# Kernel tuning notes

Hardware: AMD Instinct MI355X
Metric: run time of the kernel (lower is better)

The kernel has to match this reference:

```python
import jax, jax.numpy as jnp
import numpy as np

N = 20000   # nodes
E = 640000  # edges (avg degree 32)
D = 128     # input_nf == output_nf
H = 128     # hidden_size


def silu(x):
    return x * jax.nn.sigmoid(x)


def setup_inputs() -> dict:
    key = jax.random.key(0)
    ks = jax.random.split(key, 16)
    def lin(k, out_d, in_d, scale=None):
        s = scale if scale is not None else (1.0 / np.sqrt(in_d))
        return jax.random.uniform(k, (out_d, in_d), jnp.float32, -s, s)
    return {
        "h": jax.random.normal(ks[0], (N, D), jnp.float32),
        "coord": jax.random.normal(ks[1], (N, 3), jnp.float32),
        "edge_index": jax.random.randint(ks[2], (2, E), 0, N, jnp.int32),
        # edge_mlp: Linear(2D+1 -> H), Linear(H -> H)
        "We1": lin(ks[3], H, 2 * D + 1), "be1": jnp.zeros((H,), jnp.float32),
        "We2": lin(ks[4], H, H),          "be2": jnp.zeros((H,), jnp.float32),
        # node_mlp: Linear(H+D -> H), Linear(H -> D)
        "Wn1": lin(ks[5], H, H + D),      "bn1": jnp.zeros((H,), jnp.float32),
        "Wn2": lin(ks[6], D, H),          "bn2": jnp.zeros((D,), jnp.float32),
        # coord_mlp: Linear(H -> H), Linear(H -> 1, no bias, xavier gain=0.001)
        "Wc1": lin(ks[7], H, H),          "bc1": jnp.zeros((H,), jnp.float32),
        "Wc2": lin(ks[8], 1, H, scale=0.001 * np.sqrt(6.0 / (H + 1))),
    }


def reference(h, coord, edge_index, We1, be1, We2, be2, Wn1, bn1, Wn2, bn2, Wc1, bc1, Wc2):
    src, dst = edge_index[0], edge_index[1]

    # coord2radial (normalize=False)
    coord_diff = coord[src] - coord[dst]                 # [E, 3]
    radial = jnp.sum(coord_diff * coord_diff, axis=1, keepdims=True)  # [E, 1]

    # edge model: cat(h[src], h[dst], radial) -> Lin -> SiLU -> Lin -> SiLU
    e_in = jnp.concatenate([h[src], h[dst], radial], axis=1)  # [E, 2D+1]
    edge_feat = silu(silu(e_in @ We1.T + be1) @ We2.T + be2)  # [E, H]

    # coord model: coord_diff * coord_mlp(edge_feat), scatter-add over src
    w = silu(edge_feat @ Wc1.T + bc1) @ Wc2.T                 # [E, 1]
    trans = coord_diff * w                                    # [E, 3]
    coord_out = coord + jax.ops.segment_sum(trans, src, num_segments=N)

    # node model: agg edge_feat over src, cat(h, agg) -> Lin -> SiLU -> Lin, residual
    agg = jax.ops.segment_sum(edge_feat, src, num_segments=N)  # [N, H]
    n_in = jnp.concatenate([h, agg], axis=1)                   # [N, H+D]
    h_out = h + (silu(n_in @ Wn1.T + bn1) @ Wn2.T + bn2)       # [N, D]

    return (h_out, coord_out)
```

## Files before the change

### kernel.cpp

```cpp
#include <hip/hip_runtime.h>

#define N_NODES 20000
#define N_EDGES 640000
#define D 128
#define H 128

#define EB   128
#define TPB  512
#define NBLK 256
#define NTILE (N_EDGES / EB)
#define NNT  ((N_NODES + EB - 1) / EB)
#define ST   136

#define WS_W1   0
#define WS_W2   65536
#define WS_WC1  98304
#define WS_WN1  131072
#define WS_WN2  196608
#define WS_CNT  229376
#define WS_CUR  309376
#define WS_PERM 389376
#define WS_U    2949376
#define WS_V    8069376
#define WS_P    13189376

typedef short bf16x8 __attribute__((ext_vector_type(8)));
typedef float f32x4  __attribute__((ext_vector_type(4)));

__device__ __forceinline__ float silu_f(float x) {
    return x * __builtin_amdgcn_rcpf(1.0f + __expf(-x));
}
__device__ __forceinline__ ushort f2b(float f) {
    union { float f; unsigned int u; } v; v.f = f;
    return (ushort)((v.u + 0x7FFF + ((v.u >> 16) & 1)) >> 16);
}
__device__ __forceinline__ float b2f(ushort s) {
    union { unsigned int u; float f; } v; v.u = ((unsigned int)s) << 16; return v.f;
}

__device__ __forceinline__ void gemm_chunk_rw(const ushort* Ab, int kc0,
                                              const bf16x8 b[2], f32x4 acc[4][2],
                                              int eg, int lane)
{
    const int r = lane & 15, g = lane >> 4;
    bf16x8 a[4];
    #pragma unroll
    for (int mt = 0; mt < 4; ++mt)
        a[mt] = *(const bf16x8*)&Ab[(eg * 64 + mt * 16 + r) * ST + kc0 + g * 8];
    #pragma unroll
    for (int mt = 0; mt < 4; ++mt)
        #pragma unroll
        for (int nt = 0; nt < 2; ++nt)
            acc[mt][nt] = __builtin_amdgcn_mfma_f32_16x16x32_bf16(a[mt], b[nt], acc[mt][nt], 0, 0, 0);
}

__device__ __forceinline__ void zero_acc8(f32x4 acc[4][2]) {
    #pragma unroll
    for (int mt = 0; mt < 4; ++mt)
        #pragma unroll
        for (int nt = 0; nt < 2; ++nt)
            acc[mt][nt] = (f32x4){0.f, 0.f, 0.f, 0.f};
}

__device__ __forceinline__ void epi_silu8(f32x4 acc[4][2], const float* bias,
                                          ushort* out, int eg, int cg, int lane) {
    const int r = lane & 15, g = lane >> 4;
    #pragma unroll
    for (int nt = 0; nt < 2; ++nt) {
        int o = cg * 32 + nt * 16 + r;
        float bo = bias[o];
        #pragma unroll
        for (int mt = 0; mt < 4; ++mt)
            #pragma unroll
            for (int j = 0; j < 4; ++j) {
                int e = eg * 64 + mt * 16 + g * 4 + j;
                out[e * ST + o] = f2b(silu_f(acc[mt][nt][j] + bo));
            }
    }
}

__global__ void prep(const float* __restrict__ We1, const float* __restrict__ We2,
                     const float* __restrict__ Wc1, const float* __restrict__ Wn1,
                     const float* __restrict__ Wn2, const float* __restrict__ coord,
                     ushort* w1, ushort* w2, ushort* wc1, ushort* wn1, ushort* wn2,
                     int* cnt, float* hout, float* cout)
{
    int idx = blockIdx.x * 256 + threadIdx.x;
    if (idx < 32768) { w1[idx] = f2b(We1[(idx >> 8) * 257 + (idx & 255)]); return; }
    idx -= 32768;
    if (idx < 16384) { w2[idx] = f2b(We2[idx]); return; }
    idx -= 16384;
    if (idx < 16384) { wc1[idx] = f2b(Wc1[idx]); return; }
    idx -= 16384;
    if (idx < 32768) { wn1[idx] = f2b(Wn1[idx]); return; }
    idx -= 32768;
    if (idx < 16384) { wn2[idx] = f2b(Wn2[idx]); return; }
    idx -= 16384;
    if (idx < N_NODES) { cnt[idx] = 0; return; }
    idx -= N_NODES;
    if (idx < N_NODES * D) { hout[idx] = 0.f; return; }
    idx -= N_NODES * D;
    if (idx < N_NODES * 3) cout[idx] = coord[idx];
}

__global__ __launch_bounds__(TPB, 2)
void uvp_k(const float* __restrict__ h,
           const ushort* __restrict__ w1b, const ushort* __restrict__ wn1b,
           const float* __restrict__ be1, const float* __restrict__ bn1,
           ushort* __restrict__ u, ushort* __restrict__ v, ushort* __restrict__ p)
{
    __shared__ __align__(16) ushort hs[EB * ST];
    __shared__ float b1s[H], bn1s[H];

    const int tid = threadIdx.x, lane = tid & 63, wv = tid >> 6;
    const int eg = wv >> 2, cg = wv & 3;
    const int r = lane & 15, g = lane >> 4;
    const int n0 = blockIdx.x * EB;

    if (tid < 128) b1s[tid] = be1[tid];
    else if (tid < 256) bn1s[tid - 128] = bn1[tid - 128];

    bf16x8 wa[4][2], wb[4][2], wn[4][2];
    {
        const int c0 = cg * 32 + r, c1c = c0 + 16;
        #pragma unroll
        for (int kc = 0; kc < 4; ++kc) {
            wa[kc][0] = *(const bf16x8*)&w1b [c0  * 256 +       kc * 32 + g * 8];
            wa[kc][1] = *(const bf16x8*)&w1b [c1c * 256 +       kc * 32 + g * 8];
            wb[kc][0] = *(const bf16x8*)&w1b [c0  * 256 + 128 + kc * 32 + g * 8];
            wb[kc][1] = *(const bf16x8*)&w1b [c1c * 256 + 128 + kc * 32 + g * 8];
            wn[kc][0] = *(const bf16x8*)&wn1b[c0  * 256 +       kc * 32 + g * 8];
            wn[kc][1] = *(const bf16x8*)&wn1b[c1c * 256 +       kc * 32 + g * 8];
        }
    }
    #pragma unroll
    for (int it = 0; it < 8; ++it) {
        int idx = tid + it * TPB;
        int e = idx >> 5, c = idx & 31;
        int n = n0 + e; if (n >= N_NODES) n = 0;
        float4 vv = *(const float4*)&h[(size_t)n * D + c * 4];
        ushort4 pk; pk.x = f2b(vv.x); pk.y = f2b(vv.y); pk.z = f2b(vv.z); pk.w = f2b(vv.w);
        *(ushort4*)&hs[e * ST + c * 4] = pk;
    }
    __syncthreads();

    f32x4 acc[4][2];
    zero_acc8(acc);
    #pragma unroll
    for (int kc = 0; kc < 4; ++kc) gemm_chunk_rw(hs, kc * 32, wa[kc], acc, eg, lane);
    #pragma unroll
    for (int nt = 0; nt < 2; ++nt) {
        int o = cg * 32 + nt * 16 + r;
        float bo = b1s[o];
        #pragma unroll
        for (int mt = 0; mt < 4; ++mt)
            #pragma unroll
            for (int j = 0; j < 4; ++j) {
                int n = n0 + eg * 64 + mt * 16 + g * 4 + j;
                if (n < N_NODES) u[(size_t)n * H + o] = f2b(acc[mt][nt][j] + bo);
            }
    }
    zero_acc8(acc);
    #pragma unroll
    for (int kc = 0; kc < 4; ++kc) gemm_chunk_rw(hs, kc * 32, wb[kc], acc, eg, lane);
    #pragma unroll
    for (int nt = 0; nt < 2; ++nt) {
        int o = cg * 32 + nt * 16 + r;
        #pragma unroll
        for (int mt = 0; mt < 4; ++mt)
            #pragma unroll
            for (int j = 0; j < 4; ++j) {
                int n = n0 + eg * 64 + mt * 16 + g * 4 + j;
                if (n < N_NODES) v[(size_t)n * H + o] = f2b(acc[mt][nt][j]);
            }
    }
    zero_acc8(acc);
    #pragma unroll
    for (int kc = 0; kc < 4; ++kc) gemm_chunk_rw(hs, kc * 32, wn[kc], acc, eg, lane);
    #pragma unroll
    for (int nt = 0; nt < 2; ++nt) {
        int o = cg * 32 + nt * 16 + r;
        float bo = bn1s[o];
        #pragma unroll
        for (int mt = 0; mt < 4; ++mt)
            #pragma unroll
            for (int j = 0; j < 4; ++j) {
                int n = n0 + eg * 64 + mt * 16 + g * 4 + j;
                if (n < N_NODES) p[(size_t)n * H + o] = f2b(acc[mt][nt][j] + bo);
            }
    }
}

__global__ void hist_k(const int* __restrict__ eidx, int* cnt) {
    int e = blockIdx.x * 256 + threadIdx.x;
    if (e < N_EDGES) atomicAdd(&cnt[eidx[e]], 1);
}

__global__ void scan_k(const int* __restrict__ cnt, int* cur) {
    __shared__ int wsum[16];
    __shared__ int carry_s;
    const int t = threadIdx.x, lane = t & 63, wid = t >> 6;
    if (t == 0) carry_s = 0;
    __syncthreads();
    for (int base = 0; base < N_NODES; base += 1024) {
        int i = base + t;
        int vv = (i < N_NODES) ? cnt[i] : 0;
        int s = vv;
        #pragma unroll
        for (int d = 1; d < 64; d <<= 1) {
            int x = __shfl_up(s, d);
            if (lane >= d) s += x;
        }
        if (lane == 63) wsum[wid] = s;
        __syncthreads();
        if (wid == 0) {
            int ws = (lane < 16) ? wsum[lane] : 0;
            #pragma unroll
            for (int d = 1; d < 16; d <<= 1) {
                int x = __shfl_up(ws, d);
                if (lane >= d) ws += x;
            }
            if (lane < 16) wsum[lane] = ws;
        }
        __syncthreads();
        int woff = (wid > 0) ? wsum[wid - 1] : 0;
        if (i < N_NODES) cur[i] = carry_s + woff + s - vv;
        __syncthreads();
        if (t == 0) carry_s += wsum[15];
        __syncthreads();
    }
}

__global__ void scatter_k(const int* __restrict__ eidx, int* cur, int* perm) {
    int e = blockIdx.x * 256 + threadIdx.x;
    if (e < N_EDGES) {
        int pp = atomicAdd(&cur[eidx[e]], 1);
        perm[pp] = e;
    }
}

__global__ __launch_bounds__(TPB, 2)
void egcl_edge(const ushort* __restrict__ u, const ushort* __restrict__ v,
               const int* __restrict__ eidx, const int* __restrict__ perm,
               const float* __restrict__ coordp,
               const ushort* __restrict__ w2b, const ushort* __restrict__ wc1b,
               const float* __restrict__ We1,
               const float* __restrict__ be2, const float* __restrict__ bc1,
               const float* __restrict__ Wc2,
               float* __restrict__ agg, float* __restrict__ coord_out)
{
    __shared__ __align__(16) ushort t1[EB * ST];
    __shared__ __align__(16) ushort ef[EB * ST];
    __shared__ __align__(16) ushort c1[EB * ST];
    __shared__ int   srcs_s[2][EB], dsts_s[2][EB];
    __shared__ float radial_s[2][EB];
    __shared__ float cdx_s[2][EB], cdy_s[2][EB], cdz_s[2][EB];
    __shared__ float wco[EB], b2s[H], bc1s[H], wc2s[H];

    const int tid = threadIdx.x, lane = tid & 63, wv = tid >> 6;
    const int eg = wv >> 2, cg = wv & 3;
    const int r = lane & 15, g = lane >> 4;
    const int ce = tid >> 2, cq = tid & 3;

    if (tid < 128) b2s[tid] = be2[tid];
    else if (tid < 256) bc1s[tid - 128] = bc1[tid - 128];
    else if (tid < 384) wc2s[tid - 256] = Wc2[tid - 256];

    bf16x8 w2f[4][2], w3f[4][2];
    {
        const int c0 = cg * 32 + r, c1c = c0 + 16;
        #pragma unroll
        for (int kc = 0; kc < 4; ++kc) {
            w2f[kc][0] = *(const bf16x8*)&w2b [c0  * 128 + kc * 32 + g * 8];
            w2f[kc][1] = *(const bf16x8*)&w2b [c1c * 128 + kc * 32 + g * 8];
            w3f[kc][0] = *(const bf16x8*)&wc1b[c0  * 128 + kc * 32 + g * 8];
            w3f[kc][1] = *(const bf16x8*)&wc1b[c1c * 128 + kc * 32 + g * 8];
        }
    }
    float w256a[32];
    #pragma unroll
    for (int i = 0; i < 32; ++i) w256a[i] = We1[(cq * 32 + i) * 257 + 256];

    int t = (int)blockIdx.x;
    int rs = 0, rd = 0;
    float rsx = 0, rsy = 0, rsz = 0, rdx = 0, rdy = 0, rdz = 0;
    if (tid < EB) {
        int e = perm[t * EB + tid];
        rs = eidx[e]; rd = eidx[N_EDGES + e];
        rsx = coordp[rs * 3]; rsy = coordp[rs * 3 + 1]; rsz = coordp[rs * 3 + 2];
        rdx = coordp[rd * 3]; rdy = coordp[rd * 3 + 1]; rdz = coordp[rd * 3 + 2];
        srcs_s[0][tid] = rs; dsts_s[0][tid] = rd;
        float dx = rsx - rdx, dy = rsy - rdy, dz = rsz - rdz;
        cdx_s[0][tid] = dx; cdy_s[0][tid] = dy; cdz_s[0][tid] = dz;
        radial_s[0][tid] = dx * dx + dy * dy + dz * dz;
    }
    __syncthreads();

    bf16x8 uvr[8];
    {
        const ushort* up = u + (size_t)srcs_s[0][ce] * H + cq * 32;
        const ushort* vp = v + (size_t)dsts_s[0][ce] * H + cq * 32;
        #pragma unroll
        for (int i = 0; i < 4; ++i) {
            uvr[i]     = *(const bf16x8*)(up + i * 8);
            uvr[4 + i] = *(const bf16x8*)(vp + i * 8);
        }
    }
    {
        int tn = t + NBLK;
        rs = rd = 0; rsx = rsy = rsz = rdx = rdy = rdz = 0.f;
        if (tid < EB && tn < NTILE) {
            int e = perm[tn * EB + tid];
            rs = eidx[e]; rd = eidx[N_EDGES + e];
            rsx = coordp[rs * 3]; rsy = coordp[rs * 3 + 1]; rsz = coordp[rs * 3 + 2];
            rdx = coordp[rd * 3]; rdy = coordp[rd * 3 + 1]; rdz = coordp[rd * 3 + 2];
        }
    }

    f32x4 acc[4][2];
    int pb = 0;
    int en = 0, rs2 = 0, rd2 = 0;

    for (; t < NTILE; t += NBLK) {
        {
            float rad = radial_s[pb][ce];
            #pragma unroll
            for (int i = 0; i < 4; ++i) {
                bf16x8 uu = uvr[i], vx = uvr[4 + i];
                bf16x8 res;
                #pragma unroll
                for (int k = 0; k < 8; ++k) {
                    float x = b2f((ushort)uu[k]) + b2f((ushort)vx[k]) + rad * w256a[i * 8 + k];
                    res[k] = (short)f2b(silu_f(x));
                }
                *(bf16x8*)&t1[ce * ST + cq * 32 + i * 8] = res;
            }
        }
        if (tid < EB) {
            srcs_s[pb ^ 1][tid] = rs; dsts_s[pb ^ 1][tid] = rd;
            float dx = rsx - rdx, dy = rsy - rdy, dz = rsz - rdz;
            cdx_s[pb ^ 1][tid] = dx; cdy_s[pb ^ 1][tid] = dy; cdz_s[pb ^ 1][tid] = dz;
            radial_s[pb ^ 1][tid] = dx * dx + dy * dy + dz * dz;
        }
        __syncthreads();

        {
            const ushort* up = u + (size_t)srcs_s[pb ^ 1][ce] * H + cq * 32;
            const ushort* vp = v + (size_t)dsts_s[pb ^ 1][ce] * H + cq * 32;
            #pragma unroll
            for (int i = 0; i < 4; ++i) {
                uvr[i]     = *(const bf16x8*)(up + i * 8);
                uvr[4 + i] = *(const bf16x8*)(vp + i * 8);
            }
        }
        {
            int tn = t + 2 * NBLK;
            en = 0;
            if (tid < EB && tn < NTILE) en = perm[tn * EB + tid];
        }
        zero_acc8(acc);
        #pragma unroll
        for (int kc = 0; kc < 4; ++kc) gemm_chunk_rw(t1, kc * 32, w2f[kc], acc, eg, lane);
        epi_silu8(acc, b2s, ef, eg, cg, lane);
        __syncthreads();

        if (tid < EB) { rs2 = eidx[en]; rd2 = eidx[N_EDGES + en]; }
        zero_acc8(acc);
        #pragma unroll
        for (int kc = 0; kc < 4; ++kc) gemm_chunk_rw(ef, kc * 32, w3f[kc], acc, eg, lane);
        epi_silu8(acc, bc1s, c1, eg, cg, lane);
        __syncthreads();

        if (tid < EB) {
            rs = rs2; rd = rd2;
            rsx = coordp[rs * 3]; rsy = coordp[rs * 3 + 1]; rsz = coordp[rs * 3 + 2];
            rdx = coordp[rd * 3]; rdy = coordp[rd * 3 + 1]; rdz = coordp[rd * 3 + 2];
        }
        {
            const ushort* c1r = &c1[ce * ST + cq * 32];
            float s_ = 0.f;
            #pragma unroll
            for (int k = 0; k < 32; ++k) s_ += b2f(c1r[k]) * wc2s[cq * 32 + k];
            s_ += __shfl_down(s_, 2);
            s_ += __shfl_down(s_, 1);
            if (cq == 0) wco[ce] = s_;
        }
        __syncthreads();

        if (tid < 384) {
            int e = tid / 3, c = tid - (tid / 3) * 3;
            float cdv = (c == 0) ? cdx_s[pb][e] : (c == 1) ? cdy_s[pb][e] : cdz_s[pb][e];
            atomicAdd(&coord_out[(size_t)srcs_s[pb][e] * 3 + c], cdv * wco[e]);
        }
        {
            int o = tid & 127, q = tid >> 7;
            int base = q * 32;
            float sum = 0.f;
            int cur = srcs_s[pb][base];
            for (int k = 0; k < 32; ++k) {
                int e = base + k;
                int s = srcs_s[pb][e];
                if (s != cur) {
                    atomicAdd(&agg[(size_t)cur * D + o], sum);
                    sum = 0.f; cur = s;
                }
                sum += b2f(ef[e * ST + o]);
            }
            atomicAdd(&agg[(size_t)cur * D + o], sum);
        }
        __syncthreads();
        pb ^= 1;
    }
}

__global__ __launch_bounds__(TPB, 2)
void egcl_node(const float* __restrict__ h,
               const ushort* __restrict__ wn1b, const ushort* __restrict__ wn2b,
               const ushort* __restrict__ pArr, const float* __restrict__ bn2,
               float* __restrict__ hout )
{
    __shared__ __align__(16) ushort t1[EB * ST];
    __shared__ __align__(16) ushort t2[EB * ST];
    __shared__ float b2s[H];

    const int tid = threadIdx.x, lane = tid & 63, wv = tid >> 6;
    const int eg = wv >> 2, cg = wv & 3;
    const int r = lane & 15, g = lane >> 4;
    const int n0 = blockIdx.x * EB;

    if (tid < 128) b2s[tid] = bn2[tid];

    bf16x8 wnb[4][2], w2f[4][2];
    {
        const int c0 = cg * 32 + r, c1c = c0 + 16;
        #pragma unroll
        for (int kc = 0; kc < 4; ++kc) {
            wnb[kc][0] = *(const bf16x8*)&wn1b[c0  * 256 + 128 + kc * 32 + g * 8];
            wnb[kc][1] = *(const bf16x8*)&wn1b[c1c * 256 + 128 + kc * 32 + g * 8];
            w2f[kc][0] = *(const bf16x8*)&wn2b[c0  * 128 + kc * 32 + g * 8];
            w2f[kc][1] = *(const bf16x8*)&wn2b[c1c * 128 + kc * 32 + g * 8];
        }
    }
    #pragma unroll
    for (int it = 0; it < 8; ++it) {
        int idx = tid + it * TPB;
        int e = idx >> 5, c = idx & 31;
        int n = n0 + e; if (n >= N_NODES) n = 0;
        float4 vv = *(const float4*)&hout[(size_t)n * D + c * 4];
        ushort4 pk; pk.x = f2b(vv.x); pk.y = f2b(vv.y); pk.z = f2b(vv.z); pk.w = f2b(vv.w);
        *(ushort4*)&t1[e * ST + c * 4] = pk;
    }
    __syncthreads();

    f32x4 acc[4][2];
    zero_acc8(acc);
    #pragma unroll
    for (int kc = 0; kc < 4; ++kc) gemm_chunk_rw(t1, kc * 32, wnb[kc], acc, eg, lane);
    #pragma unroll
    for (int nt = 0; nt < 2; ++nt) {
        int o = cg * 32 + nt * 16 + r;
        #pragma unroll
        for (int mt = 0; mt < 4; ++mt)
            #pragma unroll
            for (int j = 0; j < 4; ++j) {
                int e = eg * 64 + mt * 16 + g * 4 + j;
                int n = n0 + e; if (n >= N_NODES) n = 0;
                float x = acc[mt][nt][j] + b2f(pArr[(size_t)n * H + o]);
                t2[e * ST + o] = f2b(silu_f(x));
            }
    }
    __syncthreads();

    zero_acc8(acc);
    #pragma unroll
    for (int kc = 0; kc < 4; ++kc) gemm_chunk_rw(t2, kc * 32, w2f[kc], acc, eg, lane);
    #pragma unroll
    for (int nt = 0; nt < 2; ++nt) {
        int o = cg * 32 + nt * 16 + r;
        float bo = b2s[o];
        #pragma unroll
        for (int mt = 0; mt < 4; ++mt)
            #pragma unroll
            for (int j = 0; j < 4; ++j) {
                int n = n0 + eg * 64 + mt * 16 + g * 4 + j;
                if (n < N_NODES)
                    hout[(size_t)n * D + o] = h[(size_t)n * D + o] + acc[mt][nt][j] + bo;
            }
    }
}

extern "C" void kernel_launch(void* const* d_in, const int* in_sizes, int n_in,
                              void* d_out, int out_size, void* d_ws, size_t ws_size,
                              hipStream_t stream)
{
    const float* h     = (const float*)d_in[0];
    const float* coord = (const float*)d_in[1];
    const int*   eidx  = (const int*)d_in[2];
    const float* We1 = (const float*)d_in[3];
    const float* be1 = (const float*)d_in[4];
    const float* We2 = (const float*)d_in[5];
    const float* be2 = (const float*)d_in[6];
    const float* Wn1 = (const float*)d_in[7];
    const float* bn1 = (const float*)d_in[8];
    const float* Wn2 = (const float*)d_in[9];
    const float* bn2 = (const float*)d_in[10];
    const float* Wc1 = (const float*)d_in[11];
    const float* bc1 = (const float*)d_in[12];
    const float* Wc2 = (const float*)d_in[13];

    float* hout = (float*)d_out;
    float* cout = (float*)d_out + (size_t)N_NODES * D;

    char* ws = (char*)d_ws;
    ushort* w1b  = (ushort*)(ws + WS_W1);
    ushort* w2b  = (ushort*)(ws + WS_W2);
    ushort* wc1b = (ushort*)(ws + WS_WC1);
    ushort* wn1b = (ushort*)(ws + WS_WN1);
    ushort* wn2b = (ushort*)(ws + WS_WN2);
    int* cnt  = (int*)(ws + WS_CNT);
    int* cur  = (int*)(ws + WS_CUR);
    int* perm = (int*)(ws + WS_PERM);
    ushort* uArr = (ushort*)(ws + WS_U);
    ushort* vArr = (ushort*)(ws + WS_V);
    ushort* pArr = (ushort*)(ws + WS_P);

    int prep_tot = 114688 + N_NODES + N_NODES * D + N_NODES * 3;
    prep<<<(prep_tot + 255) / 256, 256, 0, stream>>>(We1, We2, Wc1, Wn1, Wn2, coord,
                                                     w1b, w2b, wc1b, wn1b, wn2b,
                                                     cnt, hout, cout);
    uvp_k<<<NNT, TPB, 0, stream>>>(h, w1b, wn1b, be1, bn1, uArr, vArr, pArr);
    hist_k<<<(N_EDGES + 255) / 256, 256, 0, stream>>>(eidx, cnt);
    scan_k<<<1, 1024, 0, stream>>>(cnt, cur);
    scatter_k<<<(N_EDGES + 255) / 256, 256, 0, stream>>>(eidx, cur, perm);
    egcl_edge<<<NBLK, TPB, 0, stream>>>(uArr, vArr, eidx, perm, coord,
                                        w2b, wc1b, We1, be2, bc1, Wc2,
                                        hout, cout);
    egcl_node<<<NNT, TPB, 0, stream>>>(h, wn1b, wn2b, pArr, bn2, hout);
}
```

Baseline: 334.6 us.

## Restructure edge kernel for higher occupancy, fuse histogram into prep, shrink node tiles

The histogram is folded into the weight-conversion prep kernel, and the output zeroing moves to hipMemsetAsync. The edge kernel aliases the c1 buffer onto t1 to cut LDS use and targets four blocks per CU with 512 blocks over contiguous tile ranges. It also moves the radial weight column from registers to LDS, fuses the coord scatter with shuffles to drop a barrier, and adds s_setprio around the MFMA loops. The node kernels use 64-node tiles with 256 threads. These changes aim for more occupancy and fewer launches and syncs. The risks are register spills under the tighter launch bound and more atomic contention.

```diff
diff --git a/kernel.cpp b/kernel.cpp
--- a/kernel.cpp
+++ b/kernel.cpp
@@ -5,12 +5,13 @@
 #define D 128
 #define H 128
 
-#define EB   128
-#define TPB  512
-#define NBLK 256
+#define EB    128
+#define TPB   512
+#define NBLK2 512
 #define NTILE (N_EDGES / EB)
-#define NNT  ((N_NODES + EB - 1) / EB)
-#define ST   136
+#define EBN   64
+#define NNT64 ((N_NODES + EBN - 1) / EBN)
+#define ST    136
 
 #define WS_W1   0
 #define WS_W2   65536
@@ -79,43 +80,42 @@
     }
 }
 
-__global__ void prep(const float* __restrict__ We1, const float* __restrict__ We2,
-                     const float* __restrict__ Wc1, const float* __restrict__ Wn1,
-                     const float* __restrict__ Wn2, const float* __restrict__ coord,
-                     ushort* w1, ushort* w2, ushort* wc1, ushort* wn1, ushort* wn2,
-                     int* cnt, float* hout, float* cout)
+__global__ void prep2(const float* __restrict__ We1, const float* __restrict__ We2,
+                      const float* __restrict__ Wc1, const float* __restrict__ Wn1,
+                      const float* __restrict__ Wn2, const float* __restrict__ coordp,
+                      const int* __restrict__ eidx,
+                      ushort* w1, ushort* w2, ushort* wc1, ushort* wn1, ushort* wn2,
+                      float* cout, int* cnt)
 {
     int idx = blockIdx.x * 256 + threadIdx.x;
-    if (idx < 32768) { w1[idx] = f2b(We1[(idx >> 8) * 257 + (idx & 255)]); return; }
-    idx -= 32768;
-    if (idx < 16384) { w2[idx] = f2b(We2[idx]); return; }
-    idx -= 16384;
-    if (idx < 16384) { wc1[idx] = f2b(Wc1[idx]); return; }
-    idx -= 16384;
-    if (idx < 32768) { wn1[idx] = f2b(Wn1[idx]); return; }
-    idx -= 32768;
-    if (idx < 16384) { wn2[idx] = f2b(Wn2[idx]); return; }
-    idx -= 16384;
-    if (idx < N_NODES) { cnt[idx] = 0; return; }
-    idx -= N_NODES;
-    if (idx < N_NODES * D) { hout[idx] = 0.f; return; }
-    idx -= N_NODES * D;
-    if (idx < N_NODES * 3) cout[idx] = coord[idx];
-}
-
-__global__ __launch_bounds__(TPB, 2)
+    if (idx < N_EDGES) atomicAdd(&cnt[eidx[idx]], 1);
+    int j = idx;
+    if (j < 32768) { w1[j] = f2b(We1[(j >> 8) * 257 + (j & 255)]); return; }
+    j -= 32768;
+    if (j < 16384) { w2[j] = f2b(We2[j]); return; }
+    j -= 16384;
+    if (j < 16384) { wc1[j] = f2b(Wc1[j]); return; }
+    j -= 16384;
+    if (j < 32768) { wn1[j] = f2b(Wn1[j]); return; }
+    j -= 32768;
+    if (j < 16384) { wn2[j] = f2b(Wn2[j]); return; }
+    j -= 16384;
+    if (j < N_NODES * 3) cout[j] = coordp[j];
+}
+
+__global__ __launch_bounds__(256, 2)
 void uvp_k(const float* __restrict__ h,
            const ushort* __restrict__ w1b, const ushort* __restrict__ wn1b,
            const float* __restrict__ be1, const float* __restrict__ bn1,
            ushort* __restrict__ u, ushort* __restrict__ v, ushort* __restrict__ p)
 {
-    __shared__ __align__(16) ushort hs[EB * ST];
+    __shared__ __align__(16) ushort hs[EBN * ST];
     __shared__ float b1s[H], bn1s[H];
 
     const int tid = threadIdx.x, lane = tid & 63, wv = tid >> 6;
     const int eg = wv >> 2, cg = wv & 3;
     const int r = lane & 15, g = lane >> 4;
-    const int n0 = blockIdx.x * EB;
+    const int n0 = blockIdx.x * EBN;
 
     if (tid < 128) b1s[tid] = be1[tid];
     else if (tid < 256) bn1s[tid - 128] = bn1[tid - 128];
@@ -135,7 +135,7 @@
     }
     #pragma unroll
     for (int it = 0; it < 8; ++it) {
-        int idx = tid + it * TPB;
+        int idx = tid + it * 256;
         int e = idx >> 5, c = idx & 31;
         int n = n0 + e; if (n >= N_NODES) n = 0;
         float4 vv = *(const float4*)&h[(size_t)n * D + c * 4];
@@ -189,11 +189,6 @@
                 if (n < N_NODES) p[(size_t)n * H + o] = f2b(acc[mt][nt][j] + bo);
             }
     }
-}
-
-__global__ void hist_k(const int* __restrict__ eidx, int* cnt) {
-    int e = blockIdx.x * 256 + threadIdx.x;
-    if (e < N_EDGES) atomicAdd(&cnt[eidx[e]], 1);
 }
 
 __global__ void scan_k(const int* __restrict__ cnt, int* cur) {
@@ -239,7 +234,7 @@
     }
 }
 
-__global__ __launch_bounds__(TPB, 2)
+__global__ __launch_bounds__(TPB, 4)
 void egcl_edge(const ushort* __restrict__ u, const ushort* __restrict__ v,
                const int* __restrict__ eidx, const int* __restrict__ perm,
                const float* __restrict__ coordp,
@@ -251,20 +246,22 @@
 {
     __shared__ __align__(16) ushort t1[EB * ST];
     __shared__ __align__(16) ushort ef[EB * ST];
-    __shared__ __align__(16) ushort c1[EB * ST];
     __shared__ int   srcs_s[2][EB], dsts_s[2][EB];
     __shared__ float radial_s[2][EB];
     __shared__ float cdx_s[2][EB], cdy_s[2][EB], cdz_s[2][EB];
-    __shared__ float wco[EB], b2s[H], bc1s[H], wc2s[H];
+    __shared__ float b2s[H], bc1s[H], wc2s[H], w256s[H];
+
+    ushort* const c1 = t1;
 
     const int tid = threadIdx.x, lane = tid & 63, wv = tid >> 6;
     const int eg = wv >> 2, cg = wv & 3;
     const int r = lane & 15, g = lane >> 4;
     const int ce = tid >> 2, cq = tid & 3;
 
-    if (tid < 128) b2s[tid] = be2[tid];
+    if (tid < 128)      b2s[tid] = be2[tid];
     else if (tid < 256) bc1s[tid - 128] = bc1[tid - 128];
     else if (tid < 384) wc2s[tid - 256] = Wc2[tid - 256];
+    else                w256s[tid - 384] = We1[(tid - 384) * 257 + 256];
 
     bf16x8 w2f[4][2], w3f[4][2];
     {
@@ -277,20 +274,19 @@
             w3f[kc][1] = *(const bf16x8*)&wc1b[c1c * 128 + kc * 32 + g * 8];
         }
     }
-    float w256a[32];
-    #pragma unroll
-    for (int i = 0; i < 32; ++i) w256a[i] = We1[(cq * 32 + i) * 257 + 256];
-
-    int t = (int)blockIdx.x;
+
+    const int tBeg = (int)(((long long)blockIdx.x * NTILE) / NBLK2);
+    const int tEnd = (int)(((long long)(blockIdx.x + 1) * NTILE) / NBLK2);
+
     int rs = 0, rd = 0;
     float rsx = 0, rsy = 0, rsz = 0, rdx = 0, rdy = 0, rdz = 0;
     if (tid < EB) {
-        int e = perm[t * EB + tid];
-        rs = eidx[e]; rd = eidx[N_EDGES + e];
-        rsx = coordp[rs * 3]; rsy = coordp[rs * 3 + 1]; rsz = coordp[rs * 3 + 2];
-        rdx = coordp[rd * 3]; rdy = coordp[rd * 3 + 1]; rdz = coordp[rd * 3 + 2];
-        srcs_s[0][tid] = rs; dsts_s[0][tid] = rd;
-        float dx = rsx - rdx, dy = rsy - rdy, dz = rsz - rdz;
+        int e = perm[tBeg * EB + tid];
+        int s = eidx[e], d = eidx[N_EDGES + e];
+        srcs_s[0][tid] = s; dsts_s[0][tid] = d;
+        float sx = coordp[s * 3], sy = coordp[s * 3 + 1], sz = coordp[s * 3 + 2];
+        float dx0 = coordp[d * 3], dy0 = coordp[d * 3 + 1], dz0 = coordp[d * 3 + 2];
+        float dx = sx - dx0, dy = sy - dy0, dz = sz - dz0;
         cdx_s[0][tid] = dx; cdy_s[0][tid] = dy; cdz_s[0][tid] = dz;
         radial_s[0][tid] = dx * dx + dy * dy + dz * dz;
     }
@@ -306,31 +302,29 @@
             uvr[4 + i] = *(const bf16x8*)(vp + i * 8);
         }
     }
-    {
-        int tn = t + NBLK;
-        rs = rd = 0; rsx = rsy = rsz = rdx = rdy = rdz = 0.f;
-        if (tid < EB && tn < NTILE) {
-            int e = perm[tn * EB + tid];
-            rs = eidx[e]; rd = eidx[N_EDGES + e];
-            rsx = coordp[rs * 3]; rsy = coordp[rs * 3 + 1]; rsz = coordp[rs * 3 + 2];
-            rdx = coordp[rd * 3]; rdy = coordp[rd * 3 + 1]; rdz = coordp[rd * 3 + 2];
-        }
+    if (tid < EB && tBeg + 1 < NTILE) {
+        int e = perm[(tBeg + 1) * EB + tid];
+        rs = eidx[e]; rd = eidx[N_EDGES + e];
+        rsx = coordp[rs * 3]; rsy = coordp[rs * 3 + 1]; rsz = coordp[rs * 3 + 2];
+        rdx = coordp[rd * 3]; rdy = coordp[rd * 3 + 1]; rdz = coordp[rd * 3 + 2];
     }
 
     f32x4 acc[4][2];
     int pb = 0;
-    int en = 0, rs2 = 0, rd2 = 0;
-
-    for (; t < NTILE; t += NBLK) {
+
+    for (int t = tBeg; t < tEnd; ++t) {
         {
             float rad = radial_s[pb][ce];
             #pragma unroll
             for (int i = 0; i < 4; ++i) {
+                float4 wlo = *(const float4*)&w256s[cq * 32 + i * 8];
+                float4 whi = *(const float4*)&w256s[cq * 32 + i * 8 + 4];
+                float wcol[8] = {wlo.x, wlo.y, wlo.z, wlo.w, whi.x, whi.y, whi.z, whi.w};
                 bf16x8 uu = uvr[i], vx = uvr[4 + i];
                 bf16x8 res;
                 #pragma unroll
                 for (int k = 0; k < 8; ++k) {
-                    float x = b2f((ushort)uu[k]) + b2f((ushort)vx[k]) + rad * w256a[i * 8 + k];
+                    float x = b2f((ushort)uu[k]) + b2f((ushort)vx[k]) + rad * wcol[k];
                     res[k] = (short)f2b(silu_f(x));
                 }
                 *(bf16x8*)&t1[ce * ST + cq * 32 + i * 8] = res;
@@ -344,31 +338,40 @@
         }
         __syncthreads();
 
-        {
-            const ushort* up = u + (size_t)srcs_s[pb ^ 1][ce] * H + cq * 32;
-            const ushort* vp = v + (size_t)dsts_s[pb ^ 1][ce] * H + cq * 32;
-            #pragma unroll
-            for (int i = 0; i < 4; ++i) {
-                uvr[i]     = *(const bf16x8*)(up + i * 8);
-                uvr[4 + i] = *(const bf16x8*)(vp + i * 8);
-            }
-        }
-        {
-            int tn = t + 2 * NBLK;
-            en = 0;
-            if (tid < EB && tn < NTILE) en = perm[tn * EB + tid];
-        }
+        int en = 0;
+        if (tid < EB && t + 2 < NTILE) en = perm[(t + 2) * EB + tid];
         zero_acc8(acc);
+        __builtin_amdgcn_s_setprio(1);
         #pragma unroll
         for (int kc = 0; kc < 4; ++kc) gemm_chunk_rw(t1, kc * 32, w2f[kc], acc, eg, lane);
+        __builtin_amdgcn_s_setprio(0);
         epi_silu8(acc, b2s, ef, eg, cg, lane);
         __syncthreads();
 
+        int rs2 = 0, rd2 = 0;
         if (tid < EB) { rs2 = eidx[en]; rd2 = eidx[N_EDGES + en]; }
         zero_acc8(acc);
+        __builtin_amdgcn_s_setprio(1);
         #pragma unroll
         for (int kc = 0; kc < 4; ++kc) gemm_chunk_rw(ef, kc * 32, w3f[kc], acc, eg, lane);
+        __builtin_amdgcn_s_setprio(0);
         epi_silu8(acc, bc1s, c1, eg, cg, lane);
+        {
+            int o = tid & 127, q = tid >> 7;
+            int base = q * 32;
+            float sum = 0.f;
+            int curs = srcs_s[pb][base];
+            for (int k = 0; k < 32; ++k) {
+                int e = base + k;
+                int s = srcs_s[pb][e];
+                if (s != curs) {
+                    atomicAdd(&agg[(size_t)curs * D + o], sum);
+                    sum = 0.f; curs = s;
+                }
+                sum += b2f(ef[e * ST + o]);
+            }
+            atomicAdd(&agg[(size_t)curs * D + o], sum);
+        }
         __syncthreads();
 
         if (tid < EB) {
@@ -383,50 +386,40 @@
             for (int k = 0; k < 32; ++k) s_ += b2f(c1r[k]) * wc2s[cq * 32 + k];
             s_ += __shfl_down(s_, 2);
             s_ += __shfl_down(s_, 1);
-            if (cq == 0) wco[ce] = s_;
-        }
-        __syncthreads();
-
-        if (tid < 384) {
-            int e = tid / 3, c = tid - (tid / 3) * 3;
-            float cdv = (c == 0) ? cdx_s[pb][e] : (c == 1) ? cdy_s[pb][e] : cdz_s[pb][e];
-            atomicAdd(&coord_out[(size_t)srcs_s[pb][e] * 3 + c], cdv * wco[e]);
+            float wfull = __shfl(s_, lane & ~3);
+            if (cq < 3) {
+                float cdv = (cq == 0) ? cdx_s[pb][ce] : (cq == 1) ? cdy_s[pb][ce] : cdz_s[pb][ce];
+                atomicAdd(&coord_out[(size_t)srcs_s[pb][ce] * 3 + cq], cdv * wfull);
+            }
         }
         {
-            int o = tid & 127, q = tid >> 7;
-            int base = q * 32;
-            float sum = 0.f;
-            int cur = srcs_s[pb][base];
-            for (int k = 0; k < 32; ++k) {
-                int e = base + k;
-                int s = srcs_s[pb][e];
-                if (s != cur) {
-                    atomicAdd(&agg[(size_t)cur * D + o], sum);
-                    sum = 0.f; cur = s;
-                }
-                sum += b2f(ef[e * ST + o]);
-            }
-            atomicAdd(&agg[(size_t)cur * D + o], sum);
+            const ushort* up = u + (size_t)srcs_s[pb ^ 1][ce] * H + cq * 32;
+            const ushort* vp = v + (size_t)dsts_s[pb ^ 1][ce] * H + cq * 32;
+            #pragma unroll
+            for (int i = 0; i < 4; ++i) {
+                uvr[i]     = *(const bf16x8*)(up + i * 8);
+                uvr[4 + i] = *(const bf16x8*)(vp + i * 8);
+            }
         }
         __syncthreads();
         pb ^= 1;
     }
 }
 
-__global__ __launch_bounds__(TPB, 2)
+__global__ __launch_bounds__(256, 4)
 void egcl_node(const float* __restrict__ h,
                const ushort* __restrict__ wn1b, const ushort* __restrict__ wn2b,
                const ushort* __restrict__ pArr, const float* __restrict__ bn2,
                float* __restrict__ hout )
 {
-    __shared__ __align__(16) ushort t1[EB * ST];
-    __shared__ __align__(16) ushort t2[EB * ST];
+    __shared__ __align__(16) ushort t1[EBN * ST];
+    __shared__ __align__(16) ushort t2[EBN * ST];
     __shared__ float b2s[H];
 
     const int tid = threadIdx.x, lane = tid & 63, wv = tid >> 6;
     const int eg = wv >> 2, cg = wv & 3;
     const int r = lane & 15, g = lane >> 4;
-    const int n0 = blockIdx.x * EB;
+    const int n0 = blockIdx.x * EBN;
 
     if (tid < 128) b2s[tid] = bn2[tid];
 
@@ -443,7 +436,7 @@
     }
     #pragma unroll
     for (int it = 0; it < 8; ++it) {
-        int idx = tid + it * TPB;
+        int idx = tid + it * 256;
         int e = idx >> 5, c = idx & 31;
         int n = n0 + e; if (n >= N_NODES) n = 0;
         float4 vv = *(const float4*)&hout[(size_t)n * D + c * 4];
@@ -524,16 +517,15 @@
     ushort* vArr = (ushort*)(ws + WS_V);
     ushort* pArr = (ushort*)(ws + WS_P);
 
-    int prep_tot = 114688 + N_NODES + N_NODES * D + N_NODES * 3;
-    prep<<<(prep_tot + 255) / 256, 256, 0, stream>>>(We1, We2, Wc1, Wn1, Wn2, coord,
-                                                     w1b, w2b, wc1b, wn1b, wn2b,
-                                                     cnt, hout, cout);
-    uvp_k<<<NNT, TPB, 0, stream>>>(h, w1b, wn1b, be1, bn1, uArr, vArr, pArr);
-    hist_k<<<(N_EDGES + 255) / 256, 256, 0, stream>>>(eidx, cnt);
+    hipMemsetAsync(hout, 0, (size_t)N_NODES * D * sizeof(float), stream);
+    hipMemsetAsync(cnt, 0, N_NODES * sizeof(int), stream);
+    prep2<<<(N_EDGES + 255) / 256, 256, 0, stream>>>(We1, We2, Wc1, Wn1, Wn2, coord, eidx,
+                                                     w1b, w2b, wc1b, wn1b, wn2b, cout, cnt);
     scan_k<<<1, 1024, 0, stream>>>(cnt, cur);
     scatter_k<<<(N_EDGES + 255) / 256, 256, 0, stream>>>(eidx, cur, perm);
-    egcl_edge<<<NBLK, TPB, 0, stream>>>(uArr, vArr, eidx, perm, coord,
-                                        w2b, wc1b, We1, be2, bc1, Wc2,
-                                        hout, cout);
-    egcl_node<<<NNT, TPB, 0, stream>>>(h, wn1b, wn2b, pArr, bn2, hout);
-}
+    uvp_k<<<NNT64, 256, 0, stream>>>(h, w1b, wn1b, be1, bn1, uArr, vArr, pArr);
+    egcl_edge<<<NBLK2, TPB, 0, stream>>>(uArr, vArr, eidx, perm, coord,
+                                         w2b, wc1b, We1, be2, bc1, Wc2,
+                                         hout, cout);
+    egcl_node<<<NNT64, 256, 0, stream>>>(h, wn1b, wn2b, pArr, bn2, hout);
+}
```

After: 342.6 us. 2.4% more time.
